# Kernel tuning notes

Hardware: AMD Instinct MI355X
Metric: run time of the kernel (lower is better)

Reference implementation:

```python
import jax, jax.numpy as jnp
import numpy as np

N, D = 8192, 256
NUM_CLASSES = 64


def setup_inputs() -> dict:
    key = jax.random.key(0)
    k1, k2 = jax.random.split(key)
    represent = jax.random.normal(k1, (N, D), dtype=jnp.float32)
    label = jax.random.randint(k2, (N,), 0, NUM_CLASSES, dtype=jnp.int64)
    t = jnp.float32(0.1)  # temperature
    return {"represent": represent, "label": label, "t": t}


def reference(represent, label, t):
    x = represent.astype(jnp.float32)                      # [N, D]
    norms = jnp.sqrt(jnp.sum(x * x, axis=-1))              # [N]
    # pairwise cosine: (x x^T) / (||xi|| ||xj||)
    cos = (x @ x.T) / (norms[:, None] * norms[None, :])    # [N, N]
    pos_mask = label[:, None] == label[None, :]            # [N, N] bool
    e = jnp.exp(cos / t)                                   # [N, N]
    # original computes exp(mask * cos / t): masked-out entries become exp(0) = 1
    pos_pair = jnp.where(pos_mask, e, 1.0).sum(axis=-1)    # [N]
    neg_pair = jnp.where(pos_mask, 1.0, e).sum(axis=-1)    # [N]
    loss = (jnp.log(neg_pair) - jnp.log(pos_pair)).sum() / represent.shape[0]
    return loss
```

## Files before the change

### kernel.cpp

```cpp
#include <hip/hip_runtime.h>
#include <hip/hip_bf16.h>

#define N_ROWS 8192
#define DIM 256
#define NUM_CLASSES 64
#define NBLK 64
#define NTRI (NBLK * (NBLK + 1) / 2)
#define SCR_PITCH 36

typedef __bf16 bf16x8 __attribute__((ext_vector_type(8)));
typedef float f32x4 __attribute__((ext_vector_type(4)));

__device__ __forceinline__ unsigned short f2bf(float f) {
  unsigned int u = __float_as_uint(f);
  u += 0x7fffu + ((u >> 16) & 1u);
  return (unsigned short)(u >> 16);
}
__device__ __forceinline__ float bf2f(unsigned short h) {
  return __uint_as_float(((unsigned int)h) << 16);
}

__device__ __forceinline__ void gload_lds16(const unsigned short* g, unsigned short* l) {
  __builtin_amdgcn_global_load_lds(
      (const __attribute__((address_space(1))) unsigned int*)g,
      (__attribute__((address_space(3))) unsigned int*)l, 16, 0, 0);
}

__device__ __forceinline__ void tri_decode(int q, int& I, int& J) {
  int i = (int)((129.0f - sqrtf(16641.0f - 8.0f * (float)q)) * 0.5f);
  while (i * (129 - i) / 2 > q) --i;
  while ((i + 1) * (128 - i) / 2 <= q) ++i;
  I = i;
  J = i + (q - i * (129 - i) / 2);
}

__global__ void __launch_bounds__(256) prep_kernel(
    const float* __restrict__ x, const float* __restrict__ tptr,
    unsigned short* __restrict__ xb, float* __restrict__ sv,
    float* __restrict__ gsum, unsigned int* __restrict__ gcnt) {
  if (blockIdx.x == 0 && threadIdx.x == 0) { *gsum = 0.f; *gcnt = 0u; }
  const int row = blockIdx.x * 4 + (threadIdx.x >> 6);
  const int lane = threadIdx.x & 63;
  const float4 v = *reinterpret_cast<const float4*>(x + (size_t)row * DIM + lane * 4);
  const unsigned short q0 = f2bf(v.x), q1 = f2bf(v.y), q2 = f2bf(v.z), q3 = f2bf(v.w);
  const float f0 = bf2f(q0), f1 = bf2f(q1), f2 = bf2f(q2), f3 = bf2f(q3);
  float ss = f0 * f0 + f1 * f1 + f2 * f2 + f3 * f3;
  ushort4 u4; u4.x = q0; u4.y = q1; u4.z = q2; u4.w = q3;
  *reinterpret_cast<ushort4*>(xb + (size_t)row * DIM + lane * 4) = u4;
  for (int m = 32; m; m >>= 1) ss += __shfl_xor(ss, m, 64);
  if (lane == 0) sv[row] = sqrtf(1.4426950408889634f / tptr[0] / ss);
}

__global__ void __launch_bounds__(256, 3) main_kernel(
    const unsigned short* __restrict__ xb, const float* __restrict__ sv,
    const int* __restrict__ lab, float* __restrict__ part) {
  const int q = blockIdx.x;
  int I, J;
  tri_decode(q, I, J);

  __shared__ alignas(16) float scr[2][128 * SCR_PITCH];
  __shared__ float colred[2][128][2];
  __shared__ float rsv[128]; __shared__ int rlab[128];
  __shared__ float csv[128]; __shared__ int clab[128];
  unsigned short* Alds = reinterpret_cast<unsigned short*>(&scr[0][0]);
  unsigned short* Blds = reinterpret_cast<unsigned short*>(
      reinterpret_cast<char*>(&scr[0][0]) + 8192);

  const int tid = threadIdx.x;
  const int wave = tid >> 6;
  const int lane = tid & 63;
  const int quad = lane >> 4;
  const int lc = lane & 15;
  const int wrow = (wave >> 1) * 64;
  const int wcol = (wave & 1) * 64;
  const int ch = wave & 1;
  const int rowBase = I * 128;
  const int colBase = J * 128;

  f32x4 acc[4][4];
  const f32x4 zero4 = {0.f, 0.f, 0.f, 0.f};
  for (int mi = 0; mi < 4; ++mi)
    for (int ni = 0; ni < 4; ++ni) acc[mi][ni] = zero4;

  const int srow = lane >> 2;
  const int sseg = (lane & 3) * 8;

  for (int kb = 0; kb < 8; ++kb) {
    const int k0 = kb * 32;
    const unsigned short* gA =
        xb + (size_t)(rowBase + wave * 32 + srow) * DIM + k0 + sseg;
    gload_lds16(gA, &Alds[(wave * 32) * 32]);
    gload_lds16(gA + 16 * DIM, &Alds[(wave * 32 + 16) * 32]);
    const unsigned short* gB =
        xb + (size_t)(colBase + wave * 32 + srow) * DIM + k0 + sseg;
    gload_lds16(gB, &Blds[(wave * 32) * 32]);
    gload_lds16(gB + 16 * DIM, &Blds[(wave * 32 + 16) * 32]);
    __syncthreads();
    bf16x8 afr[4], bfr[4];
    for (int mi = 0; mi < 4; ++mi)
      afr[mi] = *reinterpret_cast<const bf16x8*>(
          &Alds[(wrow + mi * 16 + lc) * 32 + quad * 8]);
    for (int ni = 0; ni < 4; ++ni)
      bfr[ni] = *reinterpret_cast<const bf16x8*>(
          &Blds[(wcol + ni * 16 + lc) * 32 + quad * 8]);
    for (int mi = 0; mi < 4; ++mi)
      for (int ni = 0; ni < 4; ++ni)
        acc[mi][ni] = __builtin_amdgcn_mfma_f32_16x16x32_bf16(
            afr[mi], bfr[ni], acc[mi][ni], 0, 0, 0);
    __syncthreads();
  }

  if (tid < 128) {
    rsv[tid] = sv[rowBase + tid];
    rlab[tid] = lab[rowBase + tid];
    csv[tid] = sv[colBase + tid];
    clab[tid] = lab[colBase + tid];
  }
  __syncthreads();

  float scol[4];
  int labc[4];
#pragma unroll
  for (int ni = 0; ni < 4; ++ni) {
    scol[ni] = csv[wcol + ni * 16 + lc];
    labc[ni] = clab[wcol + ni * 16 + lc];
  }
  float ctot[4] = {0.f, 0.f, 0.f, 0.f};
  float csame[4] = {0.f, 0.f, 0.f, 0.f};

#pragma unroll
  for (int mi = 0; mi < 4; ++mi) {
#pragma unroll
    for (int r = 0; r < 4; ++r) {
      const int lr = wrow + mi * 16 + quad * 4 + r;
      const float siv = rsv[lr];
      const int li = rlab[lr];
      float st = 0.f, sm = 0.f;
#pragma unroll
      for (int ni = 0; ni < 4; ++ni) {
        const float e = exp2f(acc[mi][ni][r] * (siv * scol[ni]));
        const float em = (li == labc[ni]) ? e : 0.f;
        st += e;
        sm += em;
        ctot[ni] += e;
        csame[ni] += em;
      }
      scr[0][lr * SCR_PITCH + ch * 16 + lc] = st;
      scr[1][lr * SCR_PITCH + ch * 16 + lc] = sm;
    }
  }

  if (J > I) {
#pragma unroll
    for (int ni = 0; ni < 4; ++ni) {
      float t2 = ctot[ni] + __shfl_xor(ctot[ni], 16, 64);
      t2 += __shfl_xor(t2, 32, 64);
      float s2 = csame[ni] + __shfl_xor(csame[ni], 16, 64);
      s2 += __shfl_xor(s2, 32, 64);
      if (quad == 0) {
        colred[0][wcol + ni * 16 + lc][wave >> 1] = t2;
        colred[1][wcol + ni * 16 + lc][wave >> 1] = s2;
      }
    }
  }
  __syncthreads();

  if (tid < 128) {
    const int base = tid * SCR_PITCH;
    f32x4 a0 = {0.f, 0.f, 0.f, 0.f}, a1 = {0.f, 0.f, 0.f, 0.f};
#pragma unroll
    for (int k = 0; k < 8; ++k)
      a0 += *reinterpret_cast<const f32x4*>(&scr[0][base + 4 * k]);
#pragma unroll
    for (int k = 0; k < 8; ++k)
      a1 += *reinterpret_cast<const f32x4*>(&scr[1][base + 4 * k]);
    const float st = a0[0] + a0[1] + a0[2] + a0[3];
    const float sm = a1[0] + a1[1] + a1[2] + a1[3];
    part[(size_t)J * N_ROWS + rowBase + tid] = st;
    part[(size_t)(64 + J) * N_ROWS + rowBase + tid] = sm;
    if (J > I) {
      part[(size_t)I * N_ROWS + colBase + tid] =
          colred[0][tid][0] + colred[0][tid][1];
      part[(size_t)(64 + I) * N_ROWS + colBase + tid] =
          colred[1][tid][0] + colred[1][tid][1];
    }
  }
}

__global__ void __launch_bounds__(256) row_loss_kernel(
    const float* __restrict__ part, const int* __restrict__ lab,
    float* __restrict__ gsum, unsigned int* __restrict__ gcnt,
    float* __restrict__ out) {
  __shared__ int h[NUM_CLASSES];
  if (threadIdx.x < NUM_CLASSES) h[threadIdx.x] = 0;
  __syncthreads();
  for (int i = threadIdx.x; i < N_ROWS; i += 256) atomicAdd(&h[lab[i]], 1);
  __syncthreads();

  const int row = blockIdx.x * 256 + threadIdx.x;
  float st = 0.f, sm = 0.f;
#pragma unroll 8
  for (int b = 0; b < 64; ++b) {
    st += part[(size_t)b * N_ROWS + row];
    sm += part[(size_t)(64 + b) * N_ROWS + row];
  }
  const int c = h[lab[row]];
  const float pos = sm + (float)(N_ROWS - c);
  const float neg = (st - sm) + (float)c;
  float term = logf(neg) - logf(pos);
  for (int m = 32; m; m >>= 1) term += __shfl_xor(term, m, 64);
  __shared__ float wsum[4];
  const int lane = threadIdx.x & 63;
  const int wave = threadIdx.x >> 6;
  if (lane == 0) wsum[wave] = term;
  __syncthreads();
  if (threadIdx.x == 0) {
    const float bs = wsum[0] + wsum[1] + wsum[2] + wsum[3];
    atomicAdd(gsum, bs);
    __threadfence();
    const unsigned int t = atomicAdd(gcnt, 1u);
    if (t == (unsigned int)(N_ROWS / 256 - 1)) {
      const float total = atomicAdd(gsum, 0.0f);
      out[0] = total * (1.0f / (float)N_ROWS);
    }
  }
}

extern "C" void kernel_launch(void* const* d_in, const int* in_sizes, int n_in,
                              void* d_out, int out_size, void* d_ws, size_t ws_size,
                              hipStream_t stream) {
  const float* x = (const float*)d_in[0];
  const int* lab = (const int*)d_in[1];
  const float* t = (const float*)d_in[2];
  float* out = (float*)d_out;

  char* ws = (char*)d_ws;
  unsigned short* xb = (unsigned short*)ws;
  float* sv = (float*)(ws + (4u << 20));
  float* part = (float*)(ws + (4u << 20) + (32u << 10));
  float* gsum = (float*)(ws + (8u << 20) + (32u << 10));
  unsigned int* gcnt = (unsigned int*)(ws + (8u << 20) + (32u << 10) + 8);

  prep_kernel<<<N_ROWS / 4, 256, 0, stream>>>(x, t, xb, sv, gsum, gcnt);
  main_kernel<<<NTRI, 256, 0, stream>>>(xb, sv, lab, part);
  row_loss_kernel<<<N_ROWS / 256, 256, 0, stream>>>(part, lab, gsum, gcnt, out);
}
```

Baseline: 107.5 us.

## Load MFMA fragments directly from global memory with register double-buffering

Drops LDS staging of the A/B tiles and both per-k-step barriers. Each wave now loads its bf16x8 MFMA fragments straight from global memory into registers, prefetching the next k-slice while the current slice's MFMAs run. The row/column scale and label loads are moved ahead of the GEMM loop so they overlap with it. In exchange, fragments no longer shared through LDS are read redundantly by the two waves that need them, giving more global/L2 traffic, less coalesced 16-byte loads and higher register pressure under launch_bounds(256,3).

```diff
diff --git a/kernel.cpp b/kernel.cpp
--- a/kernel.cpp
+++ b/kernel.cpp
@@ -18,12 +18,6 @@
 }
 __device__ __forceinline__ float bf2f(unsigned short h) {
   return __uint_as_float(((unsigned int)h) << 16);
-}
-
-__device__ __forceinline__ void gload_lds16(const unsigned short* g, unsigned short* l) {
-  __builtin_amdgcn_global_load_lds(
-      (const __attribute__((address_space(1))) unsigned int*)g,
-      (__attribute__((address_space(3))) unsigned int*)l, 16, 0, 0);
 }
 
 __device__ __forceinline__ void tri_decode(int q, int& I, int& J) {
@@ -62,9 +56,6 @@
   __shared__ float colred[2][128][2];
   __shared__ float rsv[128]; __shared__ int rlab[128];
   __shared__ float csv[128]; __shared__ int clab[128];
-  unsigned short* Alds = reinterpret_cast<unsigned short*>(&scr[0][0]);
-  unsigned short* Blds = reinterpret_cast<unsigned short*>(
-      reinterpret_cast<char*>(&scr[0][0]) + 8192);
 
   const int tid = threadIdx.x;
   const int wave = tid >> 6;
@@ -77,44 +68,51 @@
   const int rowBase = I * 128;
   const int colBase = J * 128;
 
-  f32x4 acc[4][4];
-  const f32x4 zero4 = {0.f, 0.f, 0.f, 0.f};
-  for (int mi = 0; mi < 4; ++mi)
-    for (int ni = 0; ni < 4; ++ni) acc[mi][ni] = zero4;
-
-  const int srow = lane >> 2;
-  const int sseg = (lane & 3) * 8;
-
-  for (int kb = 0; kb < 8; ++kb) {
-    const int k0 = kb * 32;
-    const unsigned short* gA =
-        xb + (size_t)(rowBase + wave * 32 + srow) * DIM + k0 + sseg;
-    gload_lds16(gA, &Alds[(wave * 32) * 32]);
-    gload_lds16(gA + 16 * DIM, &Alds[(wave * 32 + 16) * 32]);
-    const unsigned short* gB =
-        xb + (size_t)(colBase + wave * 32 + srow) * DIM + k0 + sseg;
-    gload_lds16(gB, &Blds[(wave * 32) * 32]);
-    gload_lds16(gB + 16 * DIM, &Blds[(wave * 32 + 16) * 32]);
-    __syncthreads();
-    bf16x8 afr[4], bfr[4];
-    for (int mi = 0; mi < 4; ++mi)
-      afr[mi] = *reinterpret_cast<const bf16x8*>(
-          &Alds[(wrow + mi * 16 + lc) * 32 + quad * 8]);
-    for (int ni = 0; ni < 4; ++ni)
-      bfr[ni] = *reinterpret_cast<const bf16x8*>(
-          &Blds[(wcol + ni * 16 + lc) * 32 + quad * 8]);
-    for (int mi = 0; mi < 4; ++mi)
-      for (int ni = 0; ni < 4; ++ni)
-        acc[mi][ni] = __builtin_amdgcn_mfma_f32_16x16x32_bf16(
-            afr[mi], bfr[ni], acc[mi][ni], 0, 0, 0);
-    __syncthreads();
-  }
-
   if (tid < 128) {
     rsv[tid] = sv[rowBase + tid];
     rlab[tid] = lab[rowBase + tid];
     csv[tid] = sv[colBase + tid];
     clab[tid] = lab[colBase + tid];
+  }
+
+  const unsigned short* aBase =
+      xb + (size_t)(rowBase + wrow + lc) * DIM + quad * 8;
+  const unsigned short* bBase =
+      xb + (size_t)(colBase + wcol + lc) * DIM + quad * 8;
+
+  f32x4 acc[4][4];
+  const f32x4 zero4 = {0.f, 0.f, 0.f, 0.f};
+  for (int mi = 0; mi < 4; ++mi)
+    for (int ni = 0; ni < 4; ++ni) acc[mi][ni] = zero4;
+
+  bf16x8 afr[2][4], bfr[2][4];
+#pragma unroll
+  for (int mi = 0; mi < 4; ++mi)
+    afr[0][mi] = *reinterpret_cast<const bf16x8*>(aBase + mi * 16 * DIM);
+#pragma unroll
+  for (int ni = 0; ni < 4; ++ni)
+    bfr[0][ni] = *reinterpret_cast<const bf16x8*>(bBase + ni * 16 * DIM);
+
+#pragma unroll
+  for (int kb = 0; kb < 8; ++kb) {
+    const int cur = kb & 1, nxt = cur ^ 1;
+    if (kb < 7) {
+      const int ko = (kb + 1) * 32;
+#pragma unroll
+      for (int mi = 0; mi < 4; ++mi)
+        afr[nxt][mi] =
+            *reinterpret_cast<const bf16x8*>(aBase + mi * 16 * DIM + ko);
+#pragma unroll
+      for (int ni = 0; ni < 4; ++ni)
+        bfr[nxt][ni] =
+            *reinterpret_cast<const bf16x8*>(bBase + ni * 16 * DIM + ko);
+    }
+#pragma unroll
+    for (int mi = 0; mi < 4; ++mi)
+#pragma unroll
+      for (int ni = 0; ni < 4; ++ni)
+        acc[mi][ni] = __builtin_amdgcn_mfma_f32_16x16x32_bf16(
+            afr[cur][mi], bfr[cur][ni], acc[mi][ni], 0, 0, 0);
   }
   __syncthreads();
 
```

After: 146.9 us. 1.37x slower.
